# Kernel optimization log

Hardware: AMD Instinct MI355X
Metric: run time of the kernel (lower is better)

## Reference

```python
import jax, jax.numpy as jnp
import numpy as np

B, N, D, H = 8, 2048, 1024, 1024

def setup_inputs() -> dict:
    key = jax.random.key(0)
    ks = jax.random.split(key, 7)
    s = 1.0 / np.sqrt(D)
    return {
        "x": jax.random.normal(ks[0], (B, N, D), dtype=jnp.float32),
        "Wq": jax.random.uniform(ks[1], (D, H), jnp.float32, -s, s),
        "bq": jax.random.uniform(ks[2], (H,), jnp.float32, -s, s),
        "Wk": jax.random.uniform(ks[3], (D, H), jnp.float32, -s, s),
        "bk": jax.random.uniform(ks[4], (H,), jnp.float32, -s, s),
        "Wv": jax.random.uniform(ks[5], (D, H), jnp.float32, -s, s),
        "bv": jax.random.uniform(ks[6], (H,), jnp.float32, -s, s),
    }

def reference(x, Wq, bq, Wk, bk, Wv, bv):
    # q, k, v: [B, N, H]
    q = jnp.einsum('bnd,dh->bnh', x, Wq) + bq
    k = jnp.einsum('bnd,dh->bnh', x, Wk) + bk
    v = jnp.einsum('bnd,dh->bnh', x, Wv) + bv
    scale = 1.0 / jnp.sqrt(jnp.asarray(q.shape[-1], q.dtype))
    score = jnp.einsum('bqh,bkh->bqk', q, k) * scale  # [B, N, N]
    causal = jnp.tril(jnp.ones((q.shape[1], q.shape[1]), dtype=bool))
    score = jnp.where(causal, score, -jnp.inf)
    attn = jax.nn.softmax(score, axis=-1)
    # dropout p=0.0 -> identity (deterministic reference)
    return jnp.einsum('bqk,bkh->bqh', attn, v)
```

## Files before the change

### kernel.cpp

```cpp
#include <hip/hip_runtime.h>
#include <hip/hip_bf16.h>
#include <stdint.h>

#define BB 8
#define NN 2048
#define DD 1024
#define HH 1024

using f32x4 = __attribute__((ext_vector_type(4))) float;
using s16x8 = __attribute__((ext_vector_type(8))) short;

__device__ __forceinline__ short f2bf(float f){
  union { float f; uint32_t u; } v; v.f = f;
  uint32_t r = (v.u + 0x7fffu + ((v.u >> 16) & 1u)) >> 16;
  return (short)r;
}
__device__ __forceinline__ float bf2f(short s){
  union { uint32_t u; float f; } v; v.u = ((uint32_t)(uint16_t)s) << 16; return v.f;
}

#define MFMA(a,b,c) __builtin_amdgcn_mfma_f32_16x16x32_bf16((a),(b),(c),0,0,0)

#define GL16(gp, lp) __builtin_amdgcn_global_load_lds( \
    (const __attribute__((address_space(1))) void*)(gp), \
    (__attribute__((address_space(3))) void*)(lp), 16, 0, 0)

__global__ __launch_bounds__(256) void k_conv_x(const float* __restrict__ x,
                                                short* __restrict__ xb){
  int gid = blockIdx.x*256 + threadIdx.x;
  const float4* xv = (const float4*)x;
  float4 a = xv[(size_t)gid*2], b2 = xv[(size_t)gid*2+1];
  s16x8 o;
  o[0]=f2bf(a.x);  o[1]=f2bf(a.y);  o[2]=f2bf(a.z);  o[3]=f2bf(a.w);
  o[4]=f2bf(b2.x); o[5]=f2bf(b2.y); o[6]=f2bf(b2.z); o[7]=f2bf(b2.w);
  *(s16x8*)(xb + (size_t)gid*8) = o;
}

__global__ __launch_bounds__(256) void k_conv_w(const float* __restrict__ Wq,
                                                const float* __restrict__ Wk,
                                                const float* __restrict__ Wv,
                                                short* __restrict__ Wt){
  __shared__ float tile[64][65];
  int bx = blockIdx.x; int mat = bx >> 8; int ti = bx & 255;
  int d0 = (ti >> 4) << 6, h0 = (ti & 15) << 6;
  const float* W = (mat==0) ? Wq : (mat==1 ? Wk : Wv);
  int t = threadIdx.x;
  for (int i=0;i<16;i++){ int e = i*256 + t; int r = e>>6, c = e&63;
    tile[r][c] = W[(size_t)(d0+r)*HH + h0 + c]; }
  __syncthreads();
  for (int i=0;i<16;i++){ int e = i*256 + t; int r = e>>6, c = e&63;
    Wt[(size_t)(mat*HH + h0 + r)*DD + d0 + c] = f2bf(tile[c][r]); }
}

__global__ __launch_bounds__(512,2) void k_gemm(const short* __restrict__ Aw,
                                                const short* __restrict__ Bw,
                                                const float* __restrict__ bq,
                                                const float* __restrict__ bk,
                                                const float* __restrict__ bv,
                                                short* __restrict__ Qw,
                                                short* __restrict__ Kw,
                                                short* __restrict__ Vw){
  __shared__ short Al[4][256*32];
  __shared__ short Bl[4][256*32];
  const int t = threadIdx.x, l = t & 63, w = t >> 6;
  const int g = l >> 4, c = l & 15;
  const int bid = blockIdx.x;
  const int bm = (bid & 7)*8 + ((bid >> 3) & 7);
  const int bn = bid >> 6;
  const int m0 = bm << 8, c0 = bn << 8;
  const int wr = w >> 2, wc = w & 3;
  f32x4 acc[8][4] = {};

  const int sr = t >> 2, sch = t & 3;
  const int u0 = sch ^ ((sr >> 1) & 3);
  const int u1 = sch ^ (((sr + 128) >> 1) & 3);
  const short* A0 = Aw + (size_t)(m0 + sr)*DD + u0*8;
  const short* A1 = Aw + (size_t)(m0 + sr + 128)*DD + u1*8;
  const short* B0 = Bw + (size_t)(c0 + sr)*DD + u0*8;
  const short* B1 = Bw + (size_t)(c0 + sr + 128)*DD + u1*8;
  const int d0b = sr*64 + sch*16, d1b = (sr+128)*64 + sch*16;
  auto stage = [&](int kt){
    int s = kt & 3, ko = kt*32;
    GL16(A0 + ko, (char*)&Al[s][0] + d0b);
    GL16(A1 + ko, (char*)&Al[s][0] + d1b);
    GL16(B0 + ko, (char*)&Bl[s][0] + d0b);
    GL16(B1 + ko, (char*)&Bl[s][0] + d1b);
  };

  int aoff[8], boff[4];
  #pragma unroll
  for (int mi=0;mi<8;mi++){
    int row = wr*128 + mi*16 + c;
    aoff[mi] = row*32 + (g ^ ((row>>1)&3))*8;
  }
  #pragma unroll
  for (int ni=0;ni<4;ni++){
    int row = wc*64 + ni*16 + c;
    boff[ni] = row*32 + (g ^ ((row>>1)&3))*8;
  }

  auto body = [&](int kt, bool dostage){
    int s = kt & 3;
    __builtin_amdgcn_sched_barrier(0);
    __builtin_amdgcn_s_barrier();
    __builtin_amdgcn_sched_barrier(0);
    s16x8 af[8], bfr[4];
    #pragma unroll
    for (int mi=0;mi<8;mi++) af[mi] = *(const s16x8*)&Al[s][aoff[mi]];
    #pragma unroll
    for (int ni=0;ni<4;ni++) bfr[ni] = *(const s16x8*)&Bl[s][boff[ni]];
    if (dostage) stage(kt+3);
    asm volatile("s_waitcnt lgkmcnt(0)" ::: "memory");
    __builtin_amdgcn_sched_barrier(0);
    __builtin_amdgcn_s_setprio(1);
    #pragma unroll
    for (int mi=0;mi<8;mi++)
      #pragma unroll
      for (int ni=0;ni<4;ni++)
        acc[mi][ni] = MFMA(bfr[ni], af[mi], acc[mi][ni]);
    __builtin_amdgcn_s_setprio(0);
  };

  stage(0); stage(1); stage(2);
  for (int kt = 0; kt < 30; ++kt){
    asm volatile("s_waitcnt vmcnt(8)" ::: "memory");
    body(kt, kt < 29);
  }
  asm volatile("s_waitcnt vmcnt(4)" ::: "memory");
  body(30, false);
  asm volatile("s_waitcnt vmcnt(0)" ::: "memory");
  body(31, false);

  const int mat = bn >> 2;
  short* Outp = (mat==0) ? Qw : (mat==1 ? Kw : Vw);
  const float* bias = (mat==0) ? bq : (mat==1 ? bk : bv);
  #pragma unroll
  for (int ni=0;ni<4;ni++){
    int col0 = (bn & 3)*256 + wc*64 + ni*16 + g*4;
    float4 bv4 = *(const float4*)&bias[col0];
    #pragma unroll
    for (int mi=0;mi<8;mi++){
      int orow = m0 + wr*128 + mi*16 + c;
      short4 pk;
      pk.x = f2bf(acc[mi][ni][0] + bv4.x);
      pk.y = f2bf(acc[mi][ni][1] + bv4.y);
      pk.z = f2bf(acc[mi][ni][2] + bv4.z);
      pk.w = f2bf(acc[mi][ni][3] + bv4.w);
      *(short4*)&Outp[(size_t)orow*HH + col0] = pk;
    }
  }
}

__global__ __launch_bounds__(256) void k_vtrans(const short* __restrict__ Vw,
                                                short* __restrict__ Vt){
  __shared__ uint16_t tile[64][65];
  int bx = blockIdx.x; int b = bx >> 9; int rem = bx & 511;
  int n0 = (rem >> 4) << 6, h0 = (rem & 15) << 6;
  int t = threadIdx.x;
  const uint16_t* vin = (const uint16_t*)Vw;
  uint16_t* vout = (uint16_t*)Vt;
  for (int i=0;i<16;i++){ int e = i*256 + t; int r = e>>6, c = e&63;
    tile[r][c] = vin[((size_t)b*NN + n0 + r)*HH + h0 + c]; }
  __syncthreads();
  for (int i=0;i<16;i++){ int e = i*256 + t; int r = e>>6, c = e&63;
    vout[((size_t)b*HH + h0 + r)*NN + n0 + c] = tile[c][r]; }
}

__global__ __launch_bounds__(256) void k_s(const short* __restrict__ Qw,
                                           const short* __restrict__ Kw,
                                           short* __restrict__ Pp){
  __shared__ short Ql[128*32];
  __shared__ short Kl[128*32];
  const int t = threadIdx.x, l = t & 63, w = t >> 6;
  const int g = l >> 4, c = l & 15;
  int p = blockIdx.x; int b = p & 7; int ti = p >> 3;
  int tr = 0; while ((tr+1)*(tr+2)/2 <= ti) tr++;
  int tc = ti - tr*(tr+1)/2;
  const short* Aq = Qw + ((size_t)b*NN + tr*128)*HH;
  const short* Bk = Kw + ((size_t)b*NN + tc*128)*HH;
  const float SC_EXP = 0.04508422002783268f;
  const int wq = w >> 1, wk = w & 1;
  f32x4 acc[4][4] = {};

  const int srow0 = w*32 + (l >> 2), srow1 = srow0 + 16;
  const int su0 = (l & 3) ^ ((srow0 >> 1) & 3);
  const int su1 = (l & 3) ^ ((srow1 >> 1) & 3);
  const short* Qs0 = Aq + (size_t)srow0*HH + su0*8;
  const short* Qs1 = Aq + (size_t)srow1*HH + su1*8;
  const short* Ks0 = Bk + (size_t)srow0*HH + su0*8;
  const short* Ks1 = Bk + (size_t)srow1*HH + su1*8;
  const int rchunk = (g ^ ((c>>1)&3)) * 8;
  int qoff[4], koff[4];
  #pragma unroll
  for (int mi=0;mi<4;mi++) qoff[mi] = (wq*64 + mi*16 + c)*32 + rchunk;
  #pragma unroll
  for (int ni=0;ni<4;ni++) koff[ni] = (wk*64 + ni*16 + c)*32 + rchunk;

  for (int kt = 0; kt < 32; ++kt){
    int ko = kt*32;
    __syncthreads();
    GL16(Qs0 + ko, (char*)&Ql[(w*32)*32]);
    GL16(Qs1 + ko, (char*)&Ql[(w*32+16)*32]);
    GL16(Ks0 + ko, (char*)&Kl[(w*32)*32]);
    GL16(Ks1 + ko, (char*)&Kl[(w*32+16)*32]);
    __syncthreads();
    s16x8 qf[4], kf[4];
    #pragma unroll
    for (int mi=0;mi<4;mi++) qf[mi] = *(const s16x8*)&Ql[qoff[mi]];
    #pragma unroll
    for (int ni=0;ni<4;ni++) kf[ni] = *(const s16x8*)&Kl[koff[ni]];
    #pragma unroll
    for (int mi=0;mi<4;mi++)
      #pragma unroll
      for (int ni=0;ni<4;ni++)
        acc[mi][ni] = MFMA(kf[ni], qf[mi], acc[mi][ni]);
  }

  short* Pt = Pp + ((size_t)b*136 + ti)*16384;
  #pragma unroll
  for (int ni=0;ni<4;ni++){
    int pc0 = wk*64 + ni*16 + g*4;
    #pragma unroll
    for (int mi=0;mi<4;mi++){
      int pr = wq*64 + mi*16 + c;
      short4 pk;
      #pragma unroll
      for (int i=0;i<4;i++){
        bool keep = (tc*128 + pc0 + i) <= (tr*128 + pr);
        float pv = keep ? exp2f(acc[mi][ni][i]*SC_EXP) : 0.f;
        ((short*)&pk)[i] = f2bf(pv);
      }
      *(short4*)&Pt[pr*128 + pc0] = pk;
    }
  }
}

__global__ __launch_bounds__(256) void k_pv(const short* __restrict__ Pp,
                                            const short* __restrict__ Vt,
                                            float* __restrict__ out){
  __shared__ short Pl[128*32];
  __shared__ short Vl[128*32];
  const int t = threadIdx.x, l = t & 63, w = t >> 6;
  const int g = l >> 4, c = l & 15;
  int p = blockIdx.x;
  int r = p >> 8, j = p & 255;
  int tr, id;
  if      (r==0){ tr = j>>4;        id = (j&15); }
  else if (r==1){ tr = 15-(j>>4);   id = 16 + (j&15); }
  else if (r==2){ tr = (j&15);      id = 32 + (j>>4); }
  else          { tr = 15-(j&15);   id = 48 + (j>>4); }
  int b = id & 7, hc = id >> 3;
  const short* Pb = Pp + ((size_t)b*136 + tr*(tr+1)/2)*16384;
  const short* Bv = Vt + ((size_t)b*HH + hc*128)*NN;
  const int wp = w >> 1, wh = w & 1;
  f32x4 acc[4][4] = {};
  float ls[4] = {0.f,0.f,0.f,0.f};

  const int srow0 = w*32 + (l >> 2), srow1 = srow0 + 16;
  const int su0 = (l & 3) ^ ((srow0 >> 1) & 3);
  const int su1 = (l & 3) ^ ((srow1 >> 1) & 3);
  const int rchunk = (g ^ ((c>>1)&3)) * 8;
  int poff[4], voff[4];
  #pragma unroll
  for (int mi=0;mi<4;mi++) poff[mi] = (wp*64 + mi*16 + c)*32 + rchunk;
  #pragma unroll
  for (int ni=0;ni<4;ni++) voff[ni] = (wh*64 + ni*16 + c)*32 + rchunk;

  const int nst = (tr+1)*4;
  for (int kt = 0; kt < nst; ++kt){
    const short* Ps = Pb + (size_t)(kt>>2)*16384 + (kt&3)*32;
    __syncthreads();
    GL16(Ps + srow0*128 + su0*8, (char*)&Pl[(w*32)*32]);
    GL16(Ps + srow1*128 + su1*8, (char*)&Pl[(w*32+16)*32]);
    GL16(Bv + (size_t)srow0*NN + kt*32 + su0*8, (char*)&Vl[(w*32)*32]);
    GL16(Bv + (size_t)srow1*NN + kt*32 + su1*8, (char*)&Vl[(w*32+16)*32]);
    __syncthreads();
    s16x8 pf[4], vf[4];
    #pragma unroll
    for (int mi=0;mi<4;mi++) pf[mi] = *(const s16x8*)&Pl[poff[mi]];
    #pragma unroll
    for (int ni=0;ni<4;ni++) vf[ni] = *(const s16x8*)&Vl[voff[ni]];
    #pragma unroll
    for (int mi=0;mi<4;mi++)
      #pragma unroll
      for (int e=0;e<8;e++) ls[mi] += bf2f(pf[mi][e]);
    #pragma unroll
    for (int mi=0;mi<4;mi++)
      #pragma unroll
      for (int ni=0;ni<4;ni++)
        acc[mi][ni] = MFMA(vf[ni], pf[mi], acc[mi][ni]);
  }
  #pragma unroll
  for (int mi=0;mi<4;mi++){
    ls[mi] += __shfl_xor(ls[mi], 16);
    ls[mi] += __shfl_xor(ls[mi], 32);
  }
  #pragma unroll
  for (int mi=0;mi<4;mi++){
    float linv = 1.0f / ls[mi];
    int orow = tr*128 + wp*64 + mi*16 + c;
    #pragma unroll
    for (int ni=0;ni<4;ni++){
      int h0 = hc*128 + wh*64 + ni*16 + g*4;
      float4 o4;
      o4.x = acc[mi][ni][0]*linv; o4.y = acc[mi][ni][1]*linv;
      o4.z = acc[mi][ni][2]*linv; o4.w = acc[mi][ni][3]*linv;
      *(float4*)&out[((size_t)(b*NN + orow))*HH + h0] = o4;
    }
  }
}

extern "C" void kernel_launch(void* const* d_in, const int* in_sizes, int n_in,
                              void* d_out, int out_size, void* d_ws, size_t ws_size,
                              hipStream_t stream) {
  const float* x  = (const float*)d_in[0];
  const float* Wq = (const float*)d_in[1];
  const float* bq = (const float*)d_in[2];
  const float* Wk = (const float*)d_in[3];
  const float* bk = (const float*)d_in[4];
  const float* Wv = (const float*)d_in[5];
  const float* bv = (const float*)d_in[6];
  char* ws = (char*)d_ws;
  short* xb = (short*)(ws);
  short* Pp = (short*)(ws);
  short* Wt = (short*)(ws + 35651584u);
  short* Qw = (short*)(ws + 41943040u);
  short* Kw = (short*)(ws + 75497472u);
  short* Vw = (short*)(ws + 109051904u);
  short* Vt = (short*)(ws + 142606336u);

  k_conv_x<<<8192, 256, 0, stream>>>(x, xb);
  k_conv_w<<<768, 256, 0, stream>>>(Wq, Wk, Wv, Wt);
  k_gemm<<<768, 512, 0, stream>>>(xb, Wt, bq, bk, bv, Qw, Kw, Vw);
  k_vtrans<<<4096, 256, 0, stream>>>(Vw, Vt);
  k_s<<<1088, 256, 0, stream>>>(Qw, Kw, Pp);
  k_pv<<<1024, 256, 0, stream>>>(Pp, Vt, (float*)d_out);
}
```

Before: 298.9 us.

## Double-buffer LDS in score and PV kernels, relax projection GEMM waits

The score and PV kernels move from a single LDS buffer, loaded and then synchronized every k-step, to a two-stage ping-pong buffer. The next tile's global-to-LDS load is issued before computing on the current tile, and explicit vmcnt waits plus raw barriers replace __syncthreads. The projection GEMM drops its explicit lgkmcnt(0) wait and sched barrier and reorders its fragment loads, leaving LDS-read scheduling to the compiler so it can overlap with the MFMAs. This doubles LDS use per block, which may lower occupancy, and relies on the manual wait counts being correct.

```diff
diff --git a/kernel.cpp b/kernel.cpp
--- a/kernel.cpp
+++ b/kernel.cpp
@@ -104,14 +104,12 @@
     __builtin_amdgcn_sched_barrier(0);
     __builtin_amdgcn_s_barrier();
     __builtin_amdgcn_sched_barrier(0);
-    s16x8 af[8], bfr[4];
+    s16x8 bfr[4], af[8];
+    #pragma unroll
+    for (int ni=0;ni<4;ni++) bfr[ni] = *(const s16x8*)&Bl[s][boff[ni]];
     #pragma unroll
     for (int mi=0;mi<8;mi++) af[mi] = *(const s16x8*)&Al[s][aoff[mi]];
-    #pragma unroll
-    for (int ni=0;ni<4;ni++) bfr[ni] = *(const s16x8*)&Bl[s][boff[ni]];
     if (dostage) stage(kt+3);
-    asm volatile("s_waitcnt lgkmcnt(0)" ::: "memory");
-    __builtin_amdgcn_sched_barrier(0);
     __builtin_amdgcn_s_setprio(1);
     #pragma unroll
     for (int mi=0;mi<8;mi++)
@@ -169,8 +167,8 @@
 __global__ __launch_bounds__(256) void k_s(const short* __restrict__ Qw,
                                            const short* __restrict__ Kw,
                                            short* __restrict__ Pp){
-  __shared__ short Ql[128*32];
-  __shared__ short Kl[128*32];
+  __shared__ short Ql[2][128*32];
+  __shared__ short Kl[2][128*32];
   const int t = threadIdx.x, l = t & 63, w = t >> 6;
   const int g = l >> 4, c = l & 15;
   int p = blockIdx.x; int b = p & 7; int ti = p >> 3;
@@ -189,6 +187,13 @@
   const short* Qs1 = Aq + (size_t)srow1*HH + su1*8;
   const short* Ks0 = Bk + (size_t)srow0*HH + su0*8;
   const short* Ks1 = Bk + (size_t)srow1*HH + su1*8;
+  auto stage = [&](int kt){
+    int s = kt & 1, ko = kt*32;
+    GL16(Qs0 + ko, (char*)&Ql[s][(w*32)*32]);
+    GL16(Qs1 + ko, (char*)&Ql[s][(w*32+16)*32]);
+    GL16(Ks0 + ko, (char*)&Kl[s][(w*32)*32]);
+    GL16(Ks1 + ko, (char*)&Kl[s][(w*32+16)*32]);
+  };
   const int rchunk = (g ^ ((c>>1)&3)) * 8;
   int qoff[4], koff[4];
   #pragma unroll
@@ -196,24 +201,30 @@
   #pragma unroll
   for (int ni=0;ni<4;ni++) koff[ni] = (wk*64 + ni*16 + c)*32 + rchunk;
 
+  stage(0);
   for (int kt = 0; kt < 32; ++kt){
-    int ko = kt*32;
-    __syncthreads();
-    GL16(Qs0 + ko, (char*)&Ql[(w*32)*32]);
-    GL16(Qs1 + ko, (char*)&Ql[(w*32+16)*32]);
-    GL16(Ks0 + ko, (char*)&Kl[(w*32)*32]);
-    GL16(Ks1 + ko, (char*)&Kl[(w*32+16)*32]);
-    __syncthreads();
+    const int s = kt & 1;
+    if (kt < 31){
+      stage(kt+1);
+      asm volatile("s_waitcnt vmcnt(4)" ::: "memory");
+    } else {
+      asm volatile("s_waitcnt vmcnt(0)" ::: "memory");
+    }
+    __builtin_amdgcn_sched_barrier(0);
+    __builtin_amdgcn_s_barrier();
+    __builtin_amdgcn_sched_barrier(0);
     s16x8 qf[4], kf[4];
     #pragma unroll
-    for (int mi=0;mi<4;mi++) qf[mi] = *(const s16x8*)&Ql[qoff[mi]];
-    #pragma unroll
-    for (int ni=0;ni<4;ni++) kf[ni] = *(const s16x8*)&Kl[koff[ni]];
+    for (int ni=0;ni<4;ni++) kf[ni] = *(const s16x8*)&Kl[s][koff[ni]];
+    #pragma unroll
+    for (int mi=0;mi<4;mi++) qf[mi] = *(const s16x8*)&Ql[s][qoff[mi]];
     #pragma unroll
     for (int mi=0;mi<4;mi++)
       #pragma unroll
       for (int ni=0;ni<4;ni++)
         acc[mi][ni] = MFMA(kf[ni], qf[mi], acc[mi][ni]);
+    __builtin_amdgcn_sched_barrier(0);
+    __builtin_amdgcn_s_barrier();
   }
 
   short* Pt = Pp + ((size_t)b*136 + ti)*16384;
@@ -238,8 +249,8 @@
 __global__ __launch_bounds__(256) void k_pv(const short* __restrict__ Pp,
                                             const short* __restrict__ Vt,
                                             float* __restrict__ out){
-  __shared__ short Pl[128*32];
-  __shared__ short Vl[128*32];
+  __shared__ short Pl[2][128*32];
+  __shared__ short Vl[2][128*32];
   const int t = threadIdx.x, l = t & 63, w = t >> 6;
   const int g = l >> 4, c = l & 15;
   int p = blockIdx.x;
@@ -259,6 +270,14 @@
   const int srow0 = w*32 + (l >> 2), srow1 = srow0 + 16;
   const int su0 = (l & 3) ^ ((srow0 >> 1) & 3);
   const int su1 = (l & 3) ^ ((srow1 >> 1) & 3);
+  auto stage = [&](int kt){
+    int s = kt & 1;
+    const short* Ps = Pb + (size_t)(kt>>2)*16384 + (kt&3)*32;
+    GL16(Ps + srow0*128 + su0*8, (char*)&Pl[s][(w*32)*32]);
+    GL16(Ps + srow1*128 + su1*8, (char*)&Pl[s][(w*32+16)*32]);
+    GL16(Bv + (size_t)srow0*NN + kt*32 + su0*8, (char*)&Vl[s][(w*32)*32]);
+    GL16(Bv + (size_t)srow1*NN + kt*32 + su1*8, (char*)&Vl[s][(w*32+16)*32]);
+  };
   const int rchunk = (g ^ ((c>>1)&3)) * 8;
   int poff[4], voff[4];
   #pragma unroll
@@ -267,19 +286,23 @@
   for (int ni=0;ni<4;ni++) voff[ni] = (wh*64 + ni*16 + c)*32 + rchunk;
 
   const int nst = (tr+1)*4;
+  stage(0);
   for (int kt = 0; kt < nst; ++kt){
-    const short* Ps = Pb + (size_t)(kt>>2)*16384 + (kt&3)*32;
-    __syncthreads();
-    GL16(Ps + srow0*128 + su0*8, (char*)&Pl[(w*32)*32]);
-    GL16(Ps + srow1*128 + su1*8, (char*)&Pl[(w*32+16)*32]);
-    GL16(Bv + (size_t)srow0*NN + kt*32 + su0*8, (char*)&Vl[(w*32)*32]);
-    GL16(Bv + (size_t)srow1*NN + kt*32 + su1*8, (char*)&Vl[(w*32+16)*32]);
-    __syncthreads();
+    const int s = kt & 1;
+    if (kt < nst-1){
+      stage(kt+1);
+      asm volatile("s_waitcnt vmcnt(4)" ::: "memory");
+    } else {
+      asm volatile("s_waitcnt vmcnt(0)" ::: "memory");
+    }
+    __builtin_amdgcn_sched_barrier(0);
+    __builtin_amdgcn_s_barrier();
+    __builtin_amdgcn_sched_barrier(0);
     s16x8 pf[4], vf[4];
     #pragma unroll
-    for (int mi=0;mi<4;mi++) pf[mi] = *(const s16x8*)&Pl[poff[mi]];
-    #pragma unroll
-    for (int ni=0;ni<4;ni++) vf[ni] = *(const s16x8*)&Vl[voff[ni]];
+    for (int ni=0;ni<4;ni++) vf[ni] = *(const s16x8*)&Vl[s][voff[ni]];
+    #pragma unroll
+    for (int mi=0;mi<4;mi++) pf[mi] = *(const s16x8*)&Pl[s][poff[mi]];
     #pragma unroll
     for (int mi=0;mi<4;mi++)
       #pragma unroll
@@ -289,6 +312,8 @@
       #pragma unroll
       for (int ni=0;ni<4;ni++)
         acc[mi][ni] = MFMA(vf[ni], pf[mi], acc[mi][ni]);
+    __builtin_amdgcn_sched_barrier(0);
+    __builtin_amdgcn_s_barrier();
   }
   #pragma unroll
   for (int mi=0;mi<4;mi++){
```

Measured after the change: 317.3 us. 6.2% more time.

## Fuse V transpose into QKV GEMM epilogue via LDS staging

Applied to the files above, without the earlier changes.

The separate V-transpose kernel is removed. The GEMM blocks producing V now stage their bf16 tiles through reused LDS and write V already transposed into the layout the PV kernel expects. This drops one kernel launch and a full read and write of V to global memory, at the cost of a more complex epilogue with strided LDS reads. It also reorders the fragment loads and removes the explicit lgkmcnt wait and scheduling barrier before the MFMA loop, leaving wait placement to the compiler.

```diff
diff --git a/kernel.cpp b/kernel.cpp
--- a/kernel.cpp
+++ b/kernel.cpp
@@ -59,7 +59,7 @@
                                                 const float* __restrict__ bv,
                                                 short* __restrict__ Qw,
                                                 short* __restrict__ Kw,
-                                                short* __restrict__ Vw){
+                                                short* __restrict__ Vt){
   __shared__ short Al[4][256*32];
   __shared__ short Bl[4][256*32];
   const int t = threadIdx.x, l = t & 63, w = t >> 6;
@@ -104,14 +104,12 @@
     __builtin_amdgcn_sched_barrier(0);
     __builtin_amdgcn_s_barrier();
     __builtin_amdgcn_sched_barrier(0);
-    s16x8 af[8], bfr[4];
+    s16x8 bfr[4], af[8];
+    #pragma unroll
+    for (int ni=0;ni<4;ni++) bfr[ni] = *(const s16x8*)&Bl[s][boff[ni]];
     #pragma unroll
     for (int mi=0;mi<8;mi++) af[mi] = *(const s16x8*)&Al[s][aoff[mi]];
-    #pragma unroll
-    for (int ni=0;ni<4;ni++) bfr[ni] = *(const s16x8*)&Bl[s][boff[ni]];
     if (dostage) stage(kt+3);
-    asm volatile("s_waitcnt lgkmcnt(0)" ::: "memory");
-    __builtin_amdgcn_sched_barrier(0);
     __builtin_amdgcn_s_setprio(1);
     #pragma unroll
     for (int mi=0;mi<8;mi++)
@@ -132,38 +130,60 @@
   body(31, false);
 
   const int mat = bn >> 2;
-  short* Outp = (mat==0) ? Qw : (mat==1 ? Kw : Vw);
   const float* bias = (mat==0) ? bq : (mat==1 ? bk : bv);
-  #pragma unroll
-  for (int ni=0;ni<4;ni++){
-    int col0 = (bn & 3)*256 + wc*64 + ni*16 + g*4;
-    float4 bv4 = *(const float4*)&bias[col0];
-    #pragma unroll
-    for (int mi=0;mi<8;mi++){
-      int orow = m0 + wr*128 + mi*16 + c;
-      short4 pk;
-      pk.x = f2bf(acc[mi][ni][0] + bv4.x);
-      pk.y = f2bf(acc[mi][ni][1] + bv4.y);
-      pk.z = f2bf(acc[mi][ni][2] + bv4.z);
-      pk.w = f2bf(acc[mi][ni][3] + bv4.w);
-      *(short4*)&Outp[(size_t)orow*HH + col0] = pk;
+  if (mat < 2){
+    short* Outp = (mat==0) ? Qw : Kw;
+    #pragma unroll
+    for (int ni=0;ni<4;ni++){
+      int col0 = (bn & 3)*256 + wc*64 + ni*16 + g*4;
+      float4 bv4 = *(const float4*)&bias[col0];
+      #pragma unroll
+      for (int mi=0;mi<8;mi++){
+        int orow = m0 + wr*128 + mi*16 + c;
+        short4 pk;
+        pk.x = f2bf(acc[mi][ni][0] + bv4.x);
+        pk.y = f2bf(acc[mi][ni][1] + bv4.y);
+        pk.z = f2bf(acc[mi][ni][2] + bv4.z);
+        pk.w = f2bf(acc[mi][ni][3] + bv4.w);
+        *(short4*)&Outp[(size_t)orow*HH + col0] = pk;
+      }
     }
-  }
-}
-
-__global__ __launch_bounds__(256) void k_vtrans(const short* __restrict__ Vw,
-                                                short* __restrict__ Vt){
-  __shared__ uint16_t tile[64][65];
-  int bx = blockIdx.x; int b = bx >> 9; int rem = bx & 511;
-  int n0 = (rem >> 4) << 6, h0 = (rem & 15) << 6;
-  int t = threadIdx.x;
-  const uint16_t* vin = (const uint16_t*)Vw;
-  uint16_t* vout = (uint16_t*)Vt;
-  for (int i=0;i<16;i++){ int e = i*256 + t; int r = e>>6, c = e&63;
-    tile[r][c] = vin[((size_t)b*NN + n0 + r)*HH + h0 + c]; }
-  __syncthreads();
-  for (int i=0;i<16;i++){ int e = i*256 + t; int r = e>>6, c = e&63;
-    vout[((size_t)b*HH + h0 + r)*NN + n0 + c] = tile[c][r]; }
+  } else {
+    short* S = (w < 4) ? ((short*)&Al[0][0] + w*4352)
+                       : ((short*)&Bl[0][0] + (w-4)*4352);
+    const int bb = m0 >> 11;
+    const int nbase = m0 & 2047;
+    const int hglob0 = (bn & 3)*256 + wc*64;
+    #pragma unroll
+    for (int rr = 0; rr < 2; ++rr){
+      const int R = 2*wr + rr;
+      asm volatile("" ::: "memory");
+      #pragma unroll
+      for (int ni=0;ni<4;ni++){
+        int col0 = hglob0 + ni*16 + g*4;
+        float4 bv4 = *(const float4*)&bias[col0];
+        #pragma unroll
+        for (int mi2=0;mi2<4;mi2++){
+          short4 pk;
+          pk.x = f2bf(acc[rr*4+mi2][ni][0] + bv4.x);
+          pk.y = f2bf(acc[rr*4+mi2][ni][1] + bv4.y);
+          pk.z = f2bf(acc[rr*4+mi2][ni][2] + bv4.z);
+          pk.w = f2bf(acc[rr*4+mi2][ni][3] + bv4.w);
+          *(short4*)&S[(mi2*16 + c)*68 + ni*16 + g*4] = pk;
+        }
+      }
+      asm volatile("" ::: "memory");
+      #pragma unroll
+      for (int k=0;k<8;++k){
+        int hr = (l>>3) + k*8;
+        int ng = l & 7;
+        s16x8 sv;
+        #pragma unroll
+        for (int e=0;e<8;e++) sv[e] = S[(ng*8+e)*68 + hr];
+        *(s16x8*)&Vt[((size_t)bb*HH + hglob0 + hr)*NN + nbase + R*64 + ng*8] = sv;
+      }
+    }
+  }
 }
 
 __global__ __launch_bounds__(256) void k_s(const short* __restrict__ Qw,
@@ -326,13 +346,11 @@
   short* Wt = (short*)(ws + 35651584u);
   short* Qw = (short*)(ws + 41943040u);
   short* Kw = (short*)(ws + 75497472u);
-  short* Vw = (short*)(ws + 109051904u);
-  short* Vt = (short*)(ws + 142606336u);
+  short* Vt = (short*)(ws + 109051904u);
 
   k_conv_x<<<8192, 256, 0, stream>>>(x, xb);
   k_conv_w<<<768, 256, 0, stream>>>(Wq, Wk, Wv, Wt);
-  k_gemm<<<768, 512, 0, stream>>>(xb, Wt, bq, bk, bv, Qw, Kw, Vw);
-  k_vtrans<<<4096, 256, 0, stream>>>(Vw, Vt);
+  k_gemm<<<768, 512, 0, stream>>>(xb, Wt, bq, bk, bv, Qw, Kw, Vt);
   k_s<<<1088, 256, 0, stream>>>(Qw, Kw, Pp);
   k_pv<<<1024, 256, 0, stream>>>(Pp, Vt, (float*)d_out);
 }
```

Result: faster. 286.1 us (-4.3%).
